# Performance work log

Hardware: AMD Instinct MI355X
Metric: run time of the kernel (lower is better)

## Reference

```python
import jax, jax.numpy as jnp
import numpy as np

N, F_IN, F_OUT = 32768, 1024, 512
ALPHA = 0.1  # leaky relu slope


def setup_inputs() -> dict:
    key = jax.random.key(0)
    k1, k2, k3, k4, k5 = jax.random.split(key, 5)
    h = jax.random.normal(k1, (1, F_IN), dtype=jnp.float32)
    adj = jax.random.uniform(k2, (N, F_IN), dtype=jnp.float32)
    # xavier-uniform-ish init for W and a, randn for W_1 (matches torch init flavor)
    limW = float(np.sqrt(6.0 / (F_IN + F_OUT)))
    W = jax.random.uniform(k3, (F_IN, F_OUT), minval=-limW, maxval=limW, dtype=jnp.float32)
    lima = float(np.sqrt(6.0 / (2 * F_OUT + 1)))
    a = jax.random.uniform(k4, (2 * F_OUT, 1), minval=-lima, maxval=lima, dtype=jnp.float32)
    W_1 = jax.random.normal(k5, (F_IN, F_OUT), dtype=jnp.float32)
    return {"h": h, "adj": adj, "W": W, "a": a, "W_1": W_1}


def reference(h, adj, W, a, W_1):
    # W_h: [1, Fo]; W_adj: [N, Fo]
    W_h = h @ W
    W_adj = adj @ W
    # Original: cat([W_h.repeat(N,1), W_adj], dim=1) @ a.
    # Equivalent additive decomposition: (W_h @ a1) + (W_adj @ a2) -> no [N, 2Fo] intermediate.
    Fo = W.shape[1]
    a1, a2 = a[:Fo], a[Fo:]
    scores = jax.nn.leaky_relu(W_h @ a1 + W_adj @ a2, negative_slope=ALPHA).squeeze(-1)  # [N]
    attention = jax.nn.softmax(scores)  # softmax over all N rows
    W_adj_transform = adj @ W_1  # [N, Fo]
    out = attention @ W_adj_transform  # [Fo]
    # attention2 in the source: 1 where attention > mean else 0 (as an int mask)
    attention2 = (attention > attention.mean()).astype(jnp.int32)
    return out, attention2
```

## Files before the change

kernel.cpp:

```cpp
#include <hip/hip_runtime.h>

static constexpr int NROWS = 32768;
static constexpr int FIN   = 1024;
static constexpr int FOUT  = 512;
static constexpr int NREP  = 16;


__global__ __launch_bounds__(256) void k1_prep(const float* __restrict__ W,
                                               const float* __restrict__ a,
                                               const float* __restrict__ h,
                                               float* __restrict__ v,
                                               double* __restrict__ hpart) {
    const int k    = (blockIdx.x * blockDim.x + threadIdx.x) >> 6;
    const int lane = threadIdx.x & 63;

    const float4* Wrow = (const float4*)(W + (size_t)k * FOUT);
    float4 w0 = Wrow[lane];
    float4 w1 = Wrow[64 + lane];

    const float4* a4 = (const float4*)a;
    float4 a1_0 = a4[lane];
    float4 a1_1 = a4[64 + lane];
    float4 a2_0 = a4[128 + lane];
    float4 a2_1 = a4[192 + lane];

    double d1 = (double)w0.x * a1_0.x + (double)w0.y * a1_0.y +
                (double)w0.z * a1_0.z + (double)w0.w * a1_0.w +
                (double)w1.x * a1_1.x + (double)w1.y * a1_1.y +
                (double)w1.z * a1_1.z + (double)w1.w * a1_1.w;
    double d2 = (double)w0.x * a2_0.x + (double)w0.y * a2_0.y +
                (double)w0.z * a2_0.z + (double)w0.w * a2_0.w +
                (double)w1.x * a2_1.x + (double)w1.y * a2_1.y +
                (double)w1.z * a2_1.z + (double)w1.w * a2_1.w;

    #pragma unroll
    for (int off = 32; off; off >>= 1) {
        d1 += __shfl_xor(d1, off);
        d2 += __shfl_xor(d2, off);
    }
    if (lane == 0) {
        v[k]     = (float)d2;
        hpart[k] = (double)h[k] * d1;
    }
}

__global__ __launch_bounds__(256) void k2_main(const float* __restrict__ adj,
                                               const float* __restrict__ v,
                                               const double* __restrict__ hpart,
                                               double* __restrict__ e,
                                               float* __restrict__ part,
                                               double* __restrict__ zpart) {
    __shared__ float  uls[4][1024];
    __shared__ double zls[4];

    const int wave  = threadIdx.x >> 6;
    const int lane  = threadIdx.x & 63;
    const int gwave = blockIdx.x * 4 + wave;

    const int row0 = gwave * 8;
    const float4* base = (const float4*)(adj + (size_t)row0 * FIN) + lane;

    float4 R0[16], R1[16];
    #pragma unroll
    for (int r = 0; r < 4; ++r)
        #pragma unroll
        for (int q = 0; q < 4; ++q)
            R0[r * 4 + q] = base[r * 256 + q * 64];
    #pragma unroll
    for (int r = 0; r < 4; ++r)
        #pragma unroll
        for (int q = 0; q < 4; ++q)
            R1[r * 4 + q] = base[(4 + r) * 256 + q * 64];

    double c0 = 0.0;
    #pragma unroll
    for (int j = 0; j < 16; ++j) c0 += hpart[j * 64 + lane];
    #pragma unroll
    for (int off = 32; off; off >>= 1) c0 += __shfl_xor(c0, off);

    const float4* v4 = (const float4*)v;
    float4 vf[4];
    #pragma unroll
    for (int q = 0; q < 4; ++q) vf[q] = v4[q * 64 + lane];

    float  uacc[4][4] = {};
    double zacc = 0.0;

    auto do_batch4 = [&](const float4 (&buf)[16], const int rowb) {
        double d[4];
        #pragma unroll
        for (int r = 0; r < 4; ++r) {
            double dot = 0.0;
            #pragma unroll
            for (int q = 0; q < 4; ++q) {
                const float4 dd = buf[r * 4 + q];
                dot += (double)dd.x * vf[q].x + (double)dd.y * vf[q].y +
                       (double)dd.z * vf[q].z + (double)dd.w * vf[q].w;
            }
            d[r] = dot;
        }
        #pragma unroll
        for (int off = 32; off; off >>= 1) {
            #pragma unroll
            for (int r = 0; r < 4; ++r) d[r] += __shfl_xor(d[r], off);
        }

        double s[4];
        #pragma unroll
        for (int r = 0; r < 4; ++r) {
            s[r] = c0 + d[r];
            if (s[r] < 0.0) s[r] *= 0.1;
        }

        const double sx = (lane & 32) ? ((lane & 16) ? s[3] : s[2])
                                      : ((lane & 16) ? s[1] : s[0]);
        const double evx = exp(sx);
        double ev[4];
        #pragma unroll
        for (int r = 0; r < 4; ++r) ev[r] = __shfl(evx, r * 16);

        #pragma unroll
        for (int r = 0; r < 4; ++r) zacc += ev[r];
        if (lane == 0) {
            #pragma unroll
            for (int r = 0; r < 4; ++r) e[rowb + r] = ev[r];
        }

        #pragma unroll
        for (int r = 0; r < 4; ++r) {
            const float evf = (float)ev[r];
            #pragma unroll
            for (int q = 0; q < 4; ++q) {
                const float4 dd = buf[r * 4 + q];
                uacc[q][0] += evf * dd.x;
                uacc[q][1] += evf * dd.y;
                uacc[q][2] += evf * dd.z;
                uacc[q][3] += evf * dd.w;
            }
        }
    };

    do_batch4(R0, row0);
    do_batch4(R1, row0 + 4);

    float4* uls4w = (float4*)&uls[wave][0];
    #pragma unroll
    for (int q = 0; q < 4; ++q)
        uls4w[q * 64 + lane] = make_float4(uacc[q][0], uacc[q][1], uacc[q][2], uacc[q][3]);

    if (lane == 0) zls[wave] = zacc;

    __syncthreads();

    const int t = threadIdx.x;
    const float4* uls4 = (const float4*)uls;
    float4 s0 = uls4[t];
    float4 s1 = uls4[256 + t];
    float4 s2 = uls4[512 + t];
    float4 s3 = uls4[768 + t];

    float4* prow = (float4*)(part + (size_t)blockIdx.x * 1024);
    prow[t] = make_float4(s0.x + s1.x + s2.x + s3.x,
                          s0.y + s1.y + s2.y + s3.y,
                          s0.z + s1.z + s2.z + s3.z,
                          s0.w + s1.w + s2.w + s3.w);

    if (t == 0) zpart[blockIdx.x] = zls[0] + zls[1] + zls[2] + zls[3];
}

__global__ __launch_bounds__(256) void k2b_reduce(const float* __restrict__ part,
                                                  float* __restrict__ u16) {
    const int g   = blockIdx.x >> 2;
    const int c   = blockIdx.x & 3;
    const int col = c * 256 + threadIdx.x;
    const float* p = part + (size_t)g * 64 * 1024 + col;
    float acc = 0.f;
    #pragma unroll 8
    for (int b = 0; b < 64; ++b) acc += p[(size_t)b * 1024];
    u16[g * 1024 + col] = acc;
}

__device__ __forceinline__ double block_reduce_Z(const double* __restrict__ zpart,
                                                 double* zs) {
    const int t = threadIdx.x;
    zs[t] = zpart[t] + zpart[256 + t] + zpart[512 + t] + zpart[768 + t];
    __syncthreads();
    for (int st = 128; st > 0; st >>= 1) {
        if (t < st) zs[t] += zs[t + st];
        __syncthreads();
    }
    double Z = zs[0];
    __syncthreads();
    return Z;
}

__global__ __launch_bounds__(256) void k3_final(const double* __restrict__ e,
                                                const double* __restrict__ zpart,
                                                const float* __restrict__ u16,
                                                const float* __restrict__ W1,
                                                float* __restrict__ out) {
    __shared__ double zs[256];
    const double Z = block_reduce_Z(zpart, zs);
    const int t = threadIdx.x;

    if (blockIdx.x < 16) {
        __shared__ float us[1024];
        __shared__ float red[8][32];

        #pragma unroll
        for (int g = 0; g < 4; ++g) {
            const int k = g * 256 + t;
            float s = 0.f;
            #pragma unroll
            for (int rep = 0; rep < NREP; ++rep) s += u16[rep * 1024 + k];
            us[k] = s;
        }
        __syncthreads();

        const int cl  = t & 31;
        const int kg  = t >> 5;
        const int col = blockIdx.x * 32 + cl;
        float acc = 0.f;
        #pragma unroll 8
        for (int kk = 0; kk < 128; ++kk) {
            const int k = kg * 128 + kk;
            acc += us[k] * W1[(size_t)k * FOUT + col];
        }
        red[kg][cl] = acc;
        __syncthreads();
        if (t < 32) {
            float tot = 0.f;
            #pragma unroll
            for (int g = 0; g < 8; ++g) tot += red[g][t];
            out[blockIdx.x * 32 + t] = (float)((double)tot / Z);
        }
    } else {
        const int i0 = (blockIdx.x - 16) * 2048 + t * 8;
        const double2* e2 = (const double2*)(e + i0);
        const double thr = Z;
        float r[8];
        #pragma unroll
        for (int q = 0; q < 4; ++q) {
            double2 ev = e2[q];
            r[2 * q]     = (ev.x * (double)NROWS > thr) ? 1.0f : 0.0f;
            r[2 * q + 1] = (ev.y * (double)NROWS > thr) ? 1.0f : 0.0f;
        }
        float4* o4 = (float4*)(out + FOUT + i0);
        o4[0] = make_float4(r[0], r[1], r[2], r[3]);
        o4[1] = make_float4(r[4], r[5], r[6], r[7]);
    }
}

extern "C" void kernel_launch(void* const* d_in, const int* in_sizes, int n_in,
                              void* d_out, int out_size, void* d_ws, size_t ws_size,
                              hipStream_t stream) {
    const float* h   = (const float*)d_in[0];
    const float* adj = (const float*)d_in[1];
    const float* W   = (const float*)d_in[2];
    const float* a   = (const float*)d_in[3];
    const float* W1  = (const float*)d_in[4];
    float* out = (float*)d_out;

    double* e     = (double*)d_ws;
    double* hpart = e + NROWS;
    double* zpart = hpart + 1024;
    float*  v     = (float*)(zpart + 1024);
    float*  u16   = v + 1024;
    float*  part  = u16 + 16 * 1024;

    k1_prep<<<dim3(256),  dim3(256), 0, stream>>>(W, a, h, v, hpart);
    k2_main<<<dim3(1024), dim3(256), 0, stream>>>(adj, v, hpart, e, part, zpart);
    k2b_reduce<<<dim3(64), dim3(256), 0, stream>>>(part, u16);
    k3_final<<<dim3(32),  dim3(256), 0, stream>>>(e, zpart, u16, W1, out);
}
```

Before: 218.1 us.

## Stream adj rows through a double buffer instead of preloading eight rows

```diff
diff --git a/kernel.cpp b/kernel.cpp
--- a/kernel.cpp
+++ b/kernel.cpp
@@ -60,17 +60,12 @@
     const int row0 = gwave * 8;
     const float4* base = (const float4*)(adj + (size_t)row0 * FIN) + lane;
 
-    float4 R0[16], R1[16];
-    #pragma unroll
-    for (int r = 0; r < 4; ++r)
-        #pragma unroll
-        for (int q = 0; q < 4; ++q)
-            R0[r * 4 + q] = base[r * 256 + q * 64];
-    #pragma unroll
-    for (int r = 0; r < 4; ++r)
-        #pragma unroll
-        for (int q = 0; q < 4; ++q)
-            R1[r * 4 + q] = base[(4 + r) * 256 + q * 64];
+    float4 A[4], B[4];
+
+    #pragma unroll
+    for (int q = 0; q < 4; ++q) A[q] = base[q * 64];
+    #pragma unroll
+    for (int q = 0; q < 4; ++q) B[q] = base[256 + q * 64];
 
     double c0 = 0.0;
     #pragma unroll
@@ -86,62 +81,41 @@
     float  uacc[4][4] = {};
     double zacc = 0.0;
 
-    auto do_batch4 = [&](const float4 (&buf)[16], const int rowb) {
-        double d[4];
-        #pragma unroll
-        for (int r = 0; r < 4; ++r) {
-            double dot = 0.0;
+    auto do_row = [&](float4 (&buf)[4], const int r) {
+        double dot = 0.0;
+        #pragma unroll
+        for (int q = 0; q < 4; ++q) {
+            dot += (double)buf[q].x * vf[q].x + (double)buf[q].y * vf[q].y +
+                   (double)buf[q].z * vf[q].z + (double)buf[q].w * vf[q].w;
+        }
+        #pragma unroll
+        for (int off = 32; off; off >>= 1) dot += __shfl_xor(dot, off);
+
+        double s = c0 + dot;
+        if (s < 0.0) s *= 0.1;
+        const double ev = exp(s);
+        zacc += ev;
+        if (lane == 0) e[row0 + r] = ev;
+
+        const float evf = (float)ev;
+        #pragma unroll
+        for (int q = 0; q < 4; ++q) {
+            uacc[q][0] += evf * buf[q].x;
+            uacc[q][1] += evf * buf[q].y;
+            uacc[q][2] += evf * buf[q].z;
+            uacc[q][3] += evf * buf[q].w;
+        }
+
+        if (r + 2 < 8) {
             #pragma unroll
-            for (int q = 0; q < 4; ++q) {
-                const float4 dd = buf[r * 4 + q];
-                dot += (double)dd.x * vf[q].x + (double)dd.y * vf[q].y +
-                       (double)dd.z * vf[q].z + (double)dd.w * vf[q].w;
-            }
-            d[r] = dot;
-        }
-        #pragma unroll
-        for (int off = 32; off; off >>= 1) {
-            #pragma unroll
-            for (int r = 0; r < 4; ++r) d[r] += __shfl_xor(d[r], off);
-        }
-
-        double s[4];
-        #pragma unroll
-        for (int r = 0; r < 4; ++r) {
-            s[r] = c0 + d[r];
-            if (s[r] < 0.0) s[r] *= 0.1;
-        }
-
-        const double sx = (lane & 32) ? ((lane & 16) ? s[3] : s[2])
-                                      : ((lane & 16) ? s[1] : s[0]);
-        const double evx = exp(sx);
-        double ev[4];
-        #pragma unroll
-        for (int r = 0; r < 4; ++r) ev[r] = __shfl(evx, r * 16);
-
-        #pragma unroll
-        for (int r = 0; r < 4; ++r) zacc += ev[r];
-        if (lane == 0) {
-            #pragma unroll
-            for (int r = 0; r < 4; ++r) e[rowb + r] = ev[r];
-        }
-
-        #pragma unroll
-        for (int r = 0; r < 4; ++r) {
-            const float evf = (float)ev[r];
-            #pragma unroll
-            for (int q = 0; q < 4; ++q) {
-                const float4 dd = buf[r * 4 + q];
-                uacc[q][0] += evf * dd.x;
-                uacc[q][1] += evf * dd.y;
-                uacc[q][2] += evf * dd.z;
-                uacc[q][3] += evf * dd.w;
-            }
+            for (int q = 0; q < 4; ++q) buf[q] = base[(r + 2) * 256 + q * 64];
         }
     };
 
-    do_batch4(R0, row0);
-    do_batch4(R1, row0 + 4);
+    do_row(A, 0); do_row(B, 1);
+    do_row(A, 2); do_row(B, 3);
+    do_row(A, 4); do_row(B, 5);
+    do_row(A, 6); do_row(B, 7);
 
     float4* uls4w = (float4*)&uls[wave][0];
     #pragma unroll
```

Result: no change. 217.1 us (-0.5%).
